# Kernel optimization log

Hardware: AMD Instinct MI355X
Metric: run time of the kernel (lower is better)

## Reference

```python
import jax, jax.numpy as jnp
import numpy as np

N_NODES = 100000
N_EDGES = 1600000
IN_FEAT = 512
HIDDEN = 128
N_CLASSES = 7


def gcn_conv(x, edge_index, edge_weight, W, b):
    """PyG GCNConv: add self-loops (weight 1), symmetric normalization, linear, scatter-add, bias."""
    n = x.shape[0]
    src = jnp.concatenate([edge_index[0], jnp.arange(n, dtype=edge_index.dtype)])
    dst = jnp.concatenate([edge_index[1], jnp.arange(n, dtype=edge_index.dtype)])
    w = jnp.concatenate([edge_weight, jnp.ones((n,), dtype=edge_weight.dtype)])
    deg = jax.ops.segment_sum(w, dst, num_segments=n)  # degree on destination (col)
    dinv = jnp.where(deg > 0, jax.lax.rsqrt(deg), 0.0)
    norm = dinv[src] * w * dinv[dst]                   # [E+N]
    h = x @ W                                          # [N, out] transform BEFORE propagate
    msg = h[src] * norm[:, None]                       # [E+N, out] irregular gather
    out = jax.ops.segment_sum(msg, dst, num_segments=n)  # scatter-reduce
    return out + b


def setup_inputs() -> dict:
    key = jax.random.key(0)
    k1, k2, k3, k4, k5, k6 = jax.random.split(key, 6)
    x = jax.random.normal(k1, (N_NODES, IN_FEAT), dtype=jnp.float32)
    edge_index = jax.random.randint(k2, (2, N_EDGES), 0, N_NODES, dtype=jnp.int32)
    edge_weight = jax.random.uniform(k3, (N_EDGES,), dtype=jnp.float32)
    s1 = 1.0 / np.sqrt(IN_FEAT)
    s2 = 1.0 / np.sqrt(HIDDEN)
    W1 = jax.random.uniform(k4, (IN_FEAT, HIDDEN), dtype=jnp.float32, minval=-s1, maxval=s1)
    b1 = jnp.zeros((HIDDEN,), dtype=jnp.float32)
    W2 = jax.random.uniform(k5, (HIDDEN, N_CLASSES), dtype=jnp.float32, minval=-s2, maxval=s2)
    b2 = jnp.zeros((N_CLASSES,), dtype=jnp.float32)
    return {"x": x, "edge_index": edge_index, "edge_weight": edge_weight,
            "W1": W1, "b1": b1, "W2": W2, "b2": b2}


def reference(x, edge_index, edge_weight, W1, b1, W2, b2):
    # eval mode: F.dropout(training=False) is identity
    h = jax.nn.elu(gcn_conv(x, edge_index, edge_weight, W1, b1))
    out = gcn_conv(h, edge_index, edge_weight, W2, b2)
    return jax.nn.log_softmax(out, axis=1)
```

## Files before the change

kernel.cpp:

```cpp
#include <hip/hip_runtime.h>
#include <math.h>

#define N_NODES 100000
#define N_EDGES 1600000
#define IN_F 512
#define HID 128
#define NCLS 7

#define DEG_SHIFT 43
#define DEG_WMASK ((1ull << 43) - 1)
#define DEG_SCALE 4194304.0f
#define DEG_INV_SCALE (1.0f / 4194304.0f)
#define NB_SCAN 98
#define G_FILL 6250
#define G_GEMM 1563
#define G_MERGED (G_FILL + G_GEMM)

typedef short short8 __attribute__((ext_vector_type(8)));
typedef float f32x4 __attribute__((ext_vector_type(4)));
typedef unsigned long long u64;

__device__ __forceinline__ unsigned pack_bf16x2(float a, float b) {
  unsigned ua = __float_as_uint(a), ub = __float_as_uint(b);
  unsigned ra = (ua + 0x7FFFu + ((ua >> 16) & 1u)) >> 16;
  unsigned rb = (ub + 0x7FFFu + ((ub >> 16) & 1u)) >> 16;
  return ra | (rb << 16);
}
__device__ __forceinline__ unsigned short f32_to_bf16(float v) {
  unsigned u = __float_as_uint(v);
  return (unsigned short)((u + 0x7FFFu + ((u >> 16) & 1u)) >> 16);
}
__device__ __forceinline__ float bf_lo(unsigned u) { return __uint_as_float(u << 16); }
__device__ __forceinline__ float bf_hi(unsigned u) { return __uint_as_float(u & 0xFFFF0000u); }

__global__ void k_deg(const int* __restrict__ ei, const float* __restrict__ ew,
                      unsigned long long* __restrict__ packed, int* __restrict__ rank) {
  int e = blockIdx.x * 256 + threadIdx.x;
  int d = ei[N_EDGES + e];
  u64 fx = (u64)(ew[e] * DEG_SCALE + 0.5f);
  u64 old = atomicAdd(&packed[d], (1ull << DEG_SHIFT) | fx);
  rank[e] = (int)(old >> DEG_SHIFT);
}

__global__ void k_mid(const unsigned long long* __restrict__ packed,
                      float* __restrict__ dinv, int* __restrict__ cnt, int* __restrict__ bsum,
                      const float* __restrict__ W1, uint4* __restrict__ w1bf,
                      uint2* __restrict__ csr_pad) {
  const int b = blockIdx.x, t = threadIdx.x;
  if (b >= NB_SCAN) {
    int idx = (b - NB_SCAN) * 256 + t;
    if (idx < 8) csr_pad[idx] = make_uint2(0u, 0u);
    int lane = idx & 63;
    int st = idx >> 6;
    int tt = st & 7, ss = st >> 3;
    int n = tt * 16 + (lane & 15);
    int k0 = ss * 32 + (lane >> 4) * 8;
    uint4 v;
    v.x = pack_bf16x2(W1[(size_t)(k0 + 0) * HID + n], W1[(size_t)(k0 + 1) * HID + n]);
    v.y = pack_bf16x2(W1[(size_t)(k0 + 2) * HID + n], W1[(size_t)(k0 + 3) * HID + n]);
    v.z = pack_bf16x2(W1[(size_t)(k0 + 4) * HID + n], W1[(size_t)(k0 + 5) * HID + n]);
    v.w = pack_bf16x2(W1[(size_t)(k0 + 6) * HID + n], W1[(size_t)(k0 + 7) * HID + n]);
    w1bf[idx] = v;
    return;
  }
  __shared__ int sh[256];
  int base = b * 1024;
  int v = 0;
#pragma unroll
  for (int q = 0; q < 4; q++) {
    int idx = base + t * 4 + q;
    if (idx < N_NODES) {
      unsigned long long p = packed[idx];
      int c = (int)(p >> DEG_SHIFT);
      cnt[idx] = c;
      dinv[idx] = rsqrtf((float)(p & DEG_WMASK) * DEG_INV_SCALE + 1.0f);
      v += c;
    }
  }
  sh[t] = v;
  __syncthreads();
  for (int o = 128; o > 0; o >>= 1) {
    if (t < o) sh[t] += sh[t + o];
    __syncthreads();
  }
  if (t == 0) bsum[b] = sh[0];
}

__global__ void k_scan_final(const int* __restrict__ cnt, const int* __restrict__ bsum,
                             int* __restrict__ offs) {
  __shared__ int s[256];
  int t = threadIdx.x;
  int c = (t < NB_SCAN && t < blockIdx.x) ? bsum[t] : 0;
  s[t] = c;
  __syncthreads();
  for (int o = 128; o > 0; o >>= 1) {
    if (t < o) s[t] += s[t + o];
    __syncthreads();
  }
  int block_off = s[0];
  __syncthreads();
  int base = blockIdx.x * 1024;
  int v[4]; int sum = 0;
#pragma unroll
  for (int q = 0; q < 4; q++) {
    int idx = base + t * 4 + q;
    v[q] = (idx < N_NODES) ? cnt[idx] : 0;
    sum += v[q];
  }
  s[t] = sum;
  __syncthreads();
  for (int o = 1; o < 256; o <<= 1) {
    int x = (t >= o) ? s[t - o] : 0;
    __syncthreads();
    s[t] += x;
    __syncthreads();
  }
  int acc = s[t] - sum + block_off;
#pragma unroll
  for (int q = 0; q < 4; q++) {
    int idx = base + t * 4 + q;
    if (idx < N_NODES) offs[idx] = acc;
    acc += v[q];
  }
}

#define QSTR 68
__global__ __launch_bounds__(256) void k_fillgemm(
    const int* __restrict__ ei, const float* __restrict__ ew,
    const int* __restrict__ rank, const int* __restrict__ offs, uint2* __restrict__ csr,
    const float* __restrict__ x, const uint4* __restrict__ w1bf,
    const float* __restrict__ dinv, unsigned short* __restrict__ h_u16) {
  __shared__ unsigned slab[4 * 16 * QSTR];
  const int bx = blockIdx.x;
  const int tid = threadIdx.x;

  if (bx % 5 != 0) {
    int fb = bx - bx / 5 - 1;
    int e = fb * 256 + tid;
    int s = ei[e];
    int d = ei[N_EDGES + e];
    int p = offs[d] + rank[e];
    csr[p] = make_uint2((unsigned)s, __float_as_uint(ew[e]));
    return;
  }

  const int gb = bx / 5;
  const int lane = tid & 63;
  const int wv = tid >> 6;
  const int gw = gb * 4 + wv;
  if (gw >= N_NODES / 16) return;
  const int m0 = gw * 16;
  unsigned* ws = slab + wv * 16 * QSTR;
  const int l16 = lane & 15, quad = lane >> 4;
  const int l32 = lane & 31, rhalf = lane >> 5;

  f32x4 acc[8];
#pragma unroll
  for (int t = 0; t < 8; t++) acc[t] = (f32x4){0.f, 0.f, 0.f, 0.f};

#pragma unroll
  for (int q = 0; q < 4; q++) {
    float4 v[8];
#pragma unroll
    for (int i = 0; i < 8; i++) {
      int row = 2 * i + rhalf;
      v[i] = *(const float4*)(x + (size_t)(m0 + row) * IN_F + q * 128 + l32 * 4);
    }
#pragma unroll
    for (int i = 0; i < 8; i++) {
      int row = 2 * i + rhalf;
      unsigned lo = pack_bf16x2(v[i].x, v[i].y);
      unsigned hi = pack_bf16x2(v[i].z, v[i].w);
      *(uint2*)&ws[row * QSTR + l32 * 2] = make_uint2(lo, hi);
    }
    __threadfence_block();
#pragma unroll
    for (int ks = 0; ks < 4; ks++) {
      short8 af = *(const short8*)&ws[l16 * QSTR + ks * 16 + quad * 4];
      const uint4* bbase = w1bf + (size_t)(q * 4 + ks) * 8 * 64 + lane;
#pragma unroll
      for (int t = 0; t < 8; t++) {
        uint4 bv = bbase[t * 64];
        acc[t] = __builtin_amdgcn_mfma_f32_16x16x32_bf16(af, *(const short8*)&bv,
                                                         acc[t], 0, 0, 0);
      }
    }
  }
  float df[4];
#pragma unroll
  for (int r = 0; r < 4; r++) df[r] = dinv[m0 + quad * 4 + r];
#pragma unroll
  for (int t = 0; t < 8; t++)
#pragma unroll
    for (int r = 0; r < 4; r++)
      h_u16[(size_t)(m0 + quad * 4 + r) * HID + t * 16 + l16] = f32_to_bf16(acc[t][r] * df[r]);
}

__global__ __launch_bounds__(256) void k_agg1(const unsigned* __restrict__ h_u,
    const float* __restrict__ dinv, const int* __restrict__ offs, const int* __restrict__ cnt,
    const uint2* __restrict__ csr, const float* __restrict__ b1,
    const float* __restrict__ W2, float* __restrict__ h2) {
  int i = blockIdx.x * 4 + (threadIdx.x >> 6);
  int lane = threadIdx.x & 63;
  if (i >= N_NODES) return;
  float w2a[NCLS], w2b[NCLS];
#pragma unroll
  for (int c = 0; c < NCLS; c++) {
    w2a[c] = W2[(size_t)(2 * lane) * NCLS + c];
    w2b[c] = W2[(size_t)(2 * lane + 1) * NCLS + c];
  }
  int start = offs[i], len = cnt[i];
  int end = start + len;
  float ax = 0.f, ay = 0.f;
  for (int p = start; p < end; p += 8) {
    uint2 e[8];
#pragma unroll
    for (int k = 0; k < 8; k++) e[k] = csr[p + k];
    unsigned u[8];
#pragma unroll
    for (int k = 0; k < 8; k++) u[k] = h_u[(size_t)e[k].x * 64 + lane];
#pragma unroll
    for (int k = 0; k < 8; k++) {
      float n = (k == 0 || p + k < end) ? __uint_as_float(e[k].y) : 0.f;
      ax = fmaf(bf_lo(u[k]), n, ax);
      ay = fmaf(bf_hi(u[k]), n, ay);
    }
  }
  float di = dinv[i];
  unsigned u = h_u[(size_t)i * 64 + lane];
  float2 bb = *(const float2*)(b1 + lane * 2);
  float vx = fmaf(di, ax + bf_lo(u), bb.x);
  float vy = fmaf(di, ay + bf_hi(u), bb.y);
  vx = vx > 0.f ? vx : expm1f(vx);
  vy = vy > 0.f ? vy : expm1f(vy);
  float s[NCLS];
#pragma unroll
  for (int c = 0; c < NCLS; c++) s[c] = fmaf(vy, w2b[c], vx * w2a[c]);
#pragma unroll
  for (int m = 1; m < 64; m <<= 1) {
#pragma unroll
    for (int c = 0; c < NCLS; c++) s[c] += __shfl_xor(s[c], m);
  }
  if (lane < 8) {
    float v = lane == 0 ? s[0] : lane == 1 ? s[1] : lane == 2 ? s[2] :
              lane == 3 ? s[3] : lane == 4 ? s[4] : lane == 5 ? s[5] : s[6];
    h2[(size_t)i * 8 + lane] = (lane < NCLS) ? v * di : 0.f;
  }
}

__global__ __launch_bounds__(256) void k_agg2(const float* __restrict__ h2,
    const float* __restrict__ dinv, const int* __restrict__ offs, const int* __restrict__ cnt,
    const uint2* __restrict__ csr, const float* __restrict__ b2, float* __restrict__ out) {
  int tid = threadIdx.x;
  int i = blockIdx.x * 32 + (tid >> 3);
  int f = tid & 7;
  if (i >= N_NODES) return;
  int start = offs[i], len = cnt[i];
  int end = start + len;
  float acc = 0.0f;
  for (int p = start; p < end; p += 4) {
    uint2 e0 = csr[p];
    uint2 e1 = csr[p + 1];
    uint2 e2 = csr[p + 2];
    uint2 e3 = csr[p + 3];
    float v0 = h2[(size_t)e0.x * 8 + f];
    float v1 = h2[(size_t)e1.x * 8 + f];
    float v2 = h2[(size_t)e2.x * 8 + f];
    float v3 = h2[(size_t)e3.x * 8 + f];
    float n0 = __uint_as_float(e0.y);
    float n1 = (p + 1 < end) ? __uint_as_float(e1.y) : 0.f;
    float n2 = (p + 2 < end) ? __uint_as_float(e2.y) : 0.f;
    float n3 = (p + 3 < end) ? __uint_as_float(e3.y) : 0.f;
    acc = fmaf(v0, n0, acc);
    acc = fmaf(v1, n1, acc);
    acc = fmaf(v2, n2, acc);
    acc = fmaf(v3, n3, acc);
  }
  float di = dinv[i];
  float v = fmaf(di, acc + h2[(size_t)i * 8 + f], (f < NCLS) ? b2[f] : 0.0f);
  float vm = (f < NCLS) ? v : -INFINITY;
#pragma unroll
  for (int o = 1; o < 8; o <<= 1) vm = fmaxf(vm, __shfl_xor(vm, o, 8));
  float ex = (f < NCLS) ? expf(v - vm) : 0.0f;
  float s8 = ex;
#pragma unroll
  for (int o = 1; o < 8; o <<= 1) s8 += __shfl_xor(s8, o, 8);
  float lse = logf(s8);
  if (f < NCLS) out[(size_t)i * NCLS + f] = v - vm - lse;
}

extern "C" void kernel_launch(void* const* d_in, const int* in_sizes, int n_in,
                              void* d_out, int out_size, void* d_ws, size_t ws_size,
                              hipStream_t stream) {
  const float* x  = (const float*)d_in[0];
  const int*   ei = (const int*)d_in[1];
  const float* ew = (const float*)d_in[2];
  const float* W1 = (const float*)d_in[3];
  const float* b1 = (const float*)d_in[4];
  const float* W2 = (const float*)d_in[5];
  const float* b2 = (const float*)d_in[6];
  float* out = (float*)d_out;

  char* w = (char*)d_ws;
  const size_t Npad  = ((size_t)N_NODES * 4 + 255) & ~(size_t)255;
  const size_t Npad8 = ((size_t)N_NODES * 8 + 255) & ~(size_t)255;
  const size_t Epad  = ((size_t)N_EDGES * 4 + 255) & ~(size_t)255;
  size_t off = 0;
  unsigned long long* packed = (unsigned long long*)(w + off); off += Npad8;
  float*    dinv     = (float*)(w + off);    off += Npad;
  int*      cnt      = (int*)(w + off);      off += Npad;
  int*      offs     = (int*)(w + off);      off += Npad;
  int*      bsum     = (int*)(w + off);      off += 1024;
  int*      rank     = (int*)(w + off);      off += Epad;
  uint2*    csr      = (uint2*)(w + off);    off += ((size_t)(N_EDGES + 8) * 8 + 255) & ~(size_t)255;
  uint4*    w1bf     = (uint4*)(w + off);    off += (size_t)8192 * 16;
  unsigned short* h_u16 = (unsigned short*)(w + off); off += (size_t)N_NODES * HID * 2;
  float*    h2       = (float*)(w + off);    off += (size_t)N_NODES * 8 * 4;

  hipMemsetAsync(packed, 0, Npad8, stream);

  k_deg<<<N_EDGES / 256, 256, 0, stream>>>(ei, ew, packed, rank);
  k_mid<<<NB_SCAN + 32, 256, 0, stream>>>(packed, dinv, cnt, bsum, W1, w1bf, csr + N_EDGES);
  k_scan_final<<<NB_SCAN, 256, 0, stream>>>(cnt, bsum, offs);
  k_fillgemm<<<G_MERGED, 256, 0, stream>>>(ei, ew, rank, offs, csr, x, w1bf, dinv, h_u16);
  k_agg1<<<(N_NODES + 3) / 4, 256, 0, stream>>>((const unsigned*)h_u16, dinv, offs, cnt,
                                                csr, b1, W2, h2);
  k_agg2<<<N_NODES / 32, 256, 0, stream>>>(h2, dinv, offs, cnt, csr, b2, out);
}
```

Baseline: 525.2 us.

## Stage W1 tiles in LDS and load A fragments directly in fused fill-GEMM

The fused fill/GEMM kernel now runs with 512 threads. GEMM blocks cooperatively stage each bf16 W1 quarter into shared memory, so the eight waves share it instead of each wave reading B fragments from global memory. A fragments are now loaded from x straight into registers in MFMA layout and packed to bf16 in place, which removes the per-wave LDS slab round-trip. This adds block-wide barriers and doubles the block size for the fill part. Inactive tail waves are kept alive so they still reach the barriers.

Result: faster. 494.8 us (-5.8%).

```diff
diff --git a/kernel.cpp b/kernel.cpp
--- a/kernel.cpp
+++ b/kernel.cpp
@@ -12,9 +12,10 @@
 #define DEG_SCALE 4194304.0f
 #define DEG_INV_SCALE (1.0f / 4194304.0f)
 #define NB_SCAN 98
-#define G_FILL 6250
-#define G_GEMM 1563
-#define G_MERGED (G_FILL + G_GEMM)
+
+#define FILL_BLOCKS 3125
+#define GEMM_BLOCKS 782
+#define G2 (FILL_BLOCKS + GEMM_BLOCKS)
 
 typedef short short8 __attribute__((ext_vector_type(8)));
 typedef float f32x4 __attribute__((ext_vector_type(4)));
@@ -124,19 +125,18 @@
   }
 }
 
-#define QSTR 68
-__global__ __launch_bounds__(256) void k_fillgemm(
+__global__ __launch_bounds__(512) void k_fillgemm(
     const int* __restrict__ ei, const float* __restrict__ ew,
     const int* __restrict__ rank, const int* __restrict__ offs, uint2* __restrict__ csr,
     const float* __restrict__ x, const uint4* __restrict__ w1bf,
     const float* __restrict__ dinv, unsigned short* __restrict__ h_u16) {
-  __shared__ unsigned slab[4 * 16 * QSTR];
+  __shared__ uint4 lds_b[2048];
   const int bx = blockIdx.x;
   const int tid = threadIdx.x;
 
   if (bx % 5 != 0) {
     int fb = bx - bx / 5 - 1;
-    int e = fb * 256 + tid;
+    int e = fb * 512 + tid;
     int s = ei[e];
     int d = ei[N_EDGES + e];
     int p = offs[d] + rank[e];
@@ -147,53 +147,60 @@
   const int gb = bx / 5;
   const int lane = tid & 63;
   const int wv = tid >> 6;
-  const int gw = gb * 4 + wv;
-  if (gw >= N_NODES / 16) return;
+  const int gw = gb * 8 + wv;
   const int m0 = gw * 16;
-  unsigned* ws = slab + wv * 16 * QSTR;
+  const bool act = (m0 < N_NODES);
   const int l16 = lane & 15, quad = lane >> 4;
-  const int l32 = lane & 31, rhalf = lane >> 5;
+  const float* arow = x + (size_t)(m0 + l16) * IN_F + quad * 8;
 
   f32x4 acc[8];
 #pragma unroll
   for (int t = 0; t < 8; t++) acc[t] = (f32x4){0.f, 0.f, 0.f, 0.f};
 
-#pragma unroll
   for (int q = 0; q < 4; q++) {
     float4 v[8];
-#pragma unroll
-    for (int i = 0; i < 8; i++) {
-      int row = 2 * i + rhalf;
-      v[i] = *(const float4*)(x + (size_t)(m0 + row) * IN_F + q * 128 + l32 * 4);
-    }
-#pragma unroll
-    for (int i = 0; i < 8; i++) {
-      int row = 2 * i + rhalf;
-      unsigned lo = pack_bf16x2(v[i].x, v[i].y);
-      unsigned hi = pack_bf16x2(v[i].z, v[i].w);
-      *(uint2*)&ws[row * QSTR + l32 * 2] = make_uint2(lo, hi);
-    }
-    __threadfence_block();
-#pragma unroll
-    for (int ks = 0; ks < 4; ks++) {
-      short8 af = *(const short8*)&ws[l16 * QSTR + ks * 16 + quad * 4];
-      const uint4* bbase = w1bf + (size_t)(q * 4 + ks) * 8 * 64 + lane;
-#pragma unroll
-      for (int t = 0; t < 8; t++) {
-        uint4 bv = bbase[t * 64];
-        acc[t] = __builtin_amdgcn_mfma_f32_16x16x32_bf16(af, *(const short8*)&bv,
-                                                         acc[t], 0, 0, 0);
+    if (act) {
+#pragma unroll
+      for (int ks = 0; ks < 4; ks++) {
+        const float* ap = arow + q * 128 + ks * 32;
+        v[2 * ks]     = *(const float4*)ap;
+        v[2 * ks + 1] = *(const float4*)(ap + 4);
       }
     }
-  }
-  float df[4];
-#pragma unroll
-  for (int r = 0; r < 4; r++) df[r] = dinv[m0 + quad * 4 + r];
-#pragma unroll
-  for (int t = 0; t < 8; t++)
-#pragma unroll
-    for (int r = 0; r < 4; r++)
-      h_u16[(size_t)(m0 + quad * 4 + r) * HID + t * 16 + l16] = f32_to_bf16(acc[t][r] * df[r]);
+    if (q > 0) __syncthreads();
+#pragma unroll
+    for (int j = 0; j < 4; j++)
+      lds_b[tid + j * 512] = w1bf[q * 2048 + tid + j * 512];
+    __syncthreads();
+    if (act) {
+#pragma unroll
+      for (int ks = 0; ks < 4; ks++) {
+        uint4 au;
+        au.x = pack_bf16x2(v[2 * ks].x, v[2 * ks].y);
+        au.y = pack_bf16x2(v[2 * ks].z, v[2 * ks].w);
+        au.z = pack_bf16x2(v[2 * ks + 1].x, v[2 * ks + 1].y);
+        au.w = pack_bf16x2(v[2 * ks + 1].z, v[2 * ks + 1].w);
+        short8 af = *(short8*)&au;
+        const uint4* bbase = lds_b + ks * 512 + lane;
+#pragma unroll
+        for (int t = 0; t < 8; t++) {
+          uint4 bv = bbase[t * 64];
+          acc[t] = __builtin_amdgcn_mfma_f32_16x16x32_bf16(af, *(const short8*)&bv,
+                                                           acc[t], 0, 0, 0);
+        }
+      }
+    }
+  }
+  if (act) {
+    float df[4];
+#pragma unroll
+    for (int r = 0; r < 4; r++) df[r] = dinv[m0 + quad * 4 + r];
+#pragma unroll
+    for (int t = 0; t < 8; t++)
+#pragma unroll
+      for (int r = 0; r < 4; r++)
+        h_u16[(size_t)(m0 + quad * 4 + r) * HID + t * 16 + l16] = f32_to_bf16(acc[t][r] * df[r]);
+  }
 }
 
 __global__ __launch_bounds__(256) void k_agg1(const unsigned* __restrict__ h_u,
@@ -322,7 +329,7 @@
   k_deg<<<N_EDGES / 256, 256, 0, stream>>>(ei, ew, packed, rank);
   k_mid<<<NB_SCAN + 32, 256, 0, stream>>>(packed, dinv, cnt, bsum, W1, w1bf, csr + N_EDGES);
   k_scan_final<<<NB_SCAN, 256, 0, stream>>>(cnt, bsum, offs);
-  k_fillgemm<<<G_MERGED, 256, 0, stream>>>(ei, ew, rank, offs, csr, x, w1bf, dinv, h_u16);
+  k_fillgemm<<<G2, 512, 0, stream>>>(ei, ew, rank, offs, csr, x, w1bf, dinv, h_u16);
   k_agg1<<<(N_NODES + 3) / 4, 256, 0, stream>>>((const unsigned*)h_u16, dinv, offs, cnt,
                                                 csr, b1, W2, h2);
   k_agg2<<<N_NODES / 32, 256, 0, stream>>>(h2, dinv, offs, cnt, csr, b2, out);
```
